# Kernel optimization log

Hardware: AMD Instinct MI355X
Metric: run time of the kernel (lower is better)

## Reference

```python
import jax, jax.numpy as jnp
import numpy as np

LR = 0.1  # inner-loop learning rate from `param - 0.1 * grad`

D = 4096          # memory width d; key/val are (1, d) per docstring
CTX = 512         # loss_context_size: number of keys per update step


def setup_inputs() -> dict:
    key = jax.random.key(0)
    k1, k2, k3 = jax.random.split(key, 3)
    W = jax.random.normal(k1, (D, D), dtype=jnp.float32) / np.sqrt(D)
    keys = jax.random.normal(k2, (CTX, D), dtype=jnp.float32)
    vals = jax.random.normal(k3, (CTX, D), dtype=jnp.float32)
    return {"W": W, "keys": keys, "vals": vals}


def reference(W, keys, vals):
    # OneStep.forward: preds_i = functional_forward(key_i, (W,)) = key_i @ W,
    # loss = MSE(preds, vals); new_W = W - 0.1 * dloss/dW.
    # The per-key loop is batched into a single (CTX, D) x (D, D) matmul.
    def loss_fn(Wp):
        preds = keys @ Wp  # (CTX, D)
        return jnp.mean((preds - vals) ** 2)

    g = jax.grad(loss_fn)(W)
    return W - LR * g
```

## Files before the change

kernel.cpp:

```cpp
#include <hip/hip_runtime.h>
#include <hip/hip_bf16.h>


typedef __bf16 bf16_t;
typedef __bf16 bf16x8 __attribute__((ext_vector_type(8)));
typedef float f32x4 __attribute__((ext_vector_type(4)));

#define D_DIM 4096
#define CTX_N 512
#define UPD_SCALE 9.5367431640625e-8f

__device__ __forceinline__ void gld16(const bf16_t* g, bf16_t* l) {
    __builtin_amdgcn_global_load_lds(
        (const __attribute__((address_space(1))) void*)g,
        (__attribute__((address_space(3))) void*)l, 16, 0, 0);
}

__device__ __forceinline__ void t_body2(
    float* tile, const float* __restrict__ src, bf16_t* __restrict__ dstT,
    bf16_t* __restrict__ dstN, int M, int N, int bx, int by)
{
    const int tid = threadIdx.x;
    const int C0 = bx * 64, R0 = by * 64;
    const int r  = tid >> 2, cs = (tid & 3) * 16;

    const float* s = src + (size_t)(R0 + r) * N + C0 + cs;
    float f[16];
#pragma unroll
    for (int u = 0; u < 4; ++u) {
        const float4 v = ((const float4*)s)[u];
        f[4 * u + 0] = v.x; f[4 * u + 1] = v.y; f[4 * u + 2] = v.z; f[4 * u + 3] = v.w;
    }
#pragma unroll
    for (int u = 0; u < 16; ++u) tile[r * 65 + cs + u] = f[u];

    if (dstN) {
        bf16x8 v0, v1;
#pragma unroll
        for (int u = 0; u < 8; ++u) { v0[u] = (bf16_t)f[u]; v1[u] = (bf16_t)f[8 + u]; }
        bf16_t* d = dstN + (size_t)(R0 + r) * N + C0 + cs;
        *(bf16x8*)d = v0; *(bf16x8*)(d + 8) = v1;
    }
    __syncthreads();

    bf16x8 o0, o1;
#pragma unroll
    for (int u = 0; u < 8; ++u) {
        o0[u] = (bf16_t)tile[(cs + u) * 65 + r];
        o1[u] = (bf16_t)tile[(cs + 8 + u) * 65 + r];
    }
    bf16_t* d = dstT + (size_t)(C0 + r) * M + R0 + cs;
    *(bf16x8*)d = o0; *(bf16x8*)(d + 8) = o1;
}

__global__ __launch_bounds__(256) void t_all(
    const float* __restrict__ W, const float* __restrict__ K,
    const float* __restrict__ V, bf16_t* __restrict__ Wt,
    bf16_t* __restrict__ Kt, bf16_t* __restrict__ Kb, bf16_t* __restrict__ Vt)
{
    __shared__ float tile[64 * 65];
    const int y = blockIdx.y;
    if (y < 64)      t_body2(tile, W, Wt, nullptr, D_DIM, D_DIM, blockIdx.x, y);
    else if (y < 72) t_body2(tile, K, Kt, Kb,      CTX_N, D_DIM, blockIdx.x, y - 64);
    else             t_body2(tile, V, Vt, nullptr, CTX_N, D_DIM, blockIdx.x, y - 72);
}



#define K1_LOAD(AR, BR, T)                                                   \
    _Pragma("unroll")                                                        \
    for (int x = 0; x < 4; ++x) {                                            \
        AR[x] = *(const bf16x8*)(pA + (size_t)(x * 16) * D_DIM + (T) * 32);  \
        BR[x] = *(const bf16x8*)(pB + (size_t)(x * 16) * D_DIM + (T) * 32);  \
    }

#define K1_MFMA(AR, BR)                                                      \
    _Pragma("unroll")                                                        \
    for (int mi = 0; mi < 4; ++mi)                                           \
        _Pragma("unroll")                                                    \
        for (int ni = 0; ni < 4; ++ni)                                       \
            acc[mi][ni] = __builtin_amdgcn_mfma_f32_16x16x32_bf16(           \
                AR[mi], BR[ni], acc[mi][ni], 0, 0, 0);

__global__ __launch_bounds__(256) void k1_residual(
    const bf16_t* __restrict__ Wt, const bf16_t* __restrict__ Kb,
    const bf16_t* __restrict__ Vt, bf16_t* __restrict__ Rt)
{
    __shared__ __align__(16) float ep[64 * 68];

    const int tid = threadIdx.x, wave = tid >> 6, lane = tid & 63;
    const int j0 = blockIdx.x * 64, c0 = blockIdx.y * 64;
    const int l15 = lane & 15, quad = lane >> 4;
    const int kw = wave * 1024;

    f32x4 acc[4][4] = {};

    const bf16_t* pA = Wt + (size_t)(j0 + l15) * D_DIM + kw + quad * 8;
    const bf16_t* pB = Kb + (size_t)(c0 + l15) * D_DIM + kw + quad * 8;

    bf16x8 a0[4], b0[4], a1[4], b1[4], a2[4], b2[4];

    K1_LOAD(a0, b0, 0);
    K1_LOAD(a1, b1, 1);
    K1_LOAD(a2, b2, 2);
#pragma unroll 1
    for (int t = 0; t < 27; t += 3) {
        K1_MFMA(a0, b0); K1_LOAD(a0, b0, t + 3);
        K1_MFMA(a1, b1); K1_LOAD(a1, b1, t + 4);
        K1_MFMA(a2, b2); K1_LOAD(a2, b2, t + 5);
    }
    K1_MFMA(a0, b0); K1_LOAD(a0, b0, 30);
    K1_MFMA(a1, b1); K1_LOAD(a1, b1, 31);
    K1_MFMA(a2, b2);
    K1_MFMA(a0, b0);
    K1_MFMA(a1, b1);

    __syncthreads();
#pragma unroll
    for (int w = 0; w < 4; ++w) {
        if (wave == w) {
#pragma unroll
            for (int mi = 0; mi < 4; ++mi)
#pragma unroll
                for (int ni = 0; ni < 4; ++ni)
#pragma unroll
                    for (int r = 0; r < 4; ++r) {
                        const int row = mi * 16 + quad * 4 + r;
                        const int col = ni * 16 + l15;
                        if (w == 0) ep[row * 68 + col]  = acc[mi][ni][r];
                        else        ep[row * 68 + col] += acc[mi][ni][r];
                    }
        }
        __syncthreads();
    }

    {
        const int row = tid >> 2, cs = (tid & 3) * 16;
        const size_t rbase = (size_t)(j0 + row) * CTX_N + c0 + cs;
        float e[16];
#pragma unroll
        for (int u = 0; u < 4; ++u) {
            const float4 v = ((const float4*)(ep + row * 68 + cs))[u];
            e[4 * u + 0] = v.x; e[4 * u + 1] = v.y;
            e[4 * u + 2] = v.z; e[4 * u + 3] = v.w;
        }
        const bf16x8 v0 = *(const bf16x8*)(Vt + rbase);
        const bf16x8 v1 = *(const bf16x8*)(Vt + rbase + 8);
        bf16x8 o0, o1;
#pragma unroll
        for (int u = 0; u < 8; ++u) {
            o0[u] = (bf16_t)(e[u]     - (float)v0[u]);
            o1[u] = (bf16_t)(e[8 + u] - (float)v1[u]);
        }
        *(bf16x8*)(Rt + rbase)     = o0;
        *(bf16x8*)(Rt + rbase + 8) = o1;
    }
}


#define K2_COMPUTE(BSEL)                                                     \
    {                                                                        \
        const bf16_t* As = (const bf16_t*)(smem + (BSEL) * 16384);           \
        const bf16_t* Bs = (const bf16_t*)(smem + (BSEL) * 16384 + 8192);    \
        bf16x8 af[4], bq[4];                                                 \
        _Pragma("unroll")                                                    \
        for (int mi = 0; mi < 4; ++mi)                                       \
            af[mi] = *(const bf16x8*)(As + (wi + mi * 16 + l15) * 32 + quad * 8); \
        _Pragma("unroll")                                                    \
        for (int ni = 0; ni < 4; ++ni)                                       \
            bq[ni] = *(const bf16x8*)(Bs + (wj + ni * 16 + l15) * 32 + quad * 8); \
        _Pragma("unroll")                                                    \
        for (int mi = 0; mi < 4; ++mi)                                       \
            _Pragma("unroll")                                                \
            for (int ni = 0; ni < 4; ++ni)                                   \
                acc[mi][ni] = __builtin_amdgcn_mfma_f32_16x16x32_bf16(       \
                    af[mi], bq[ni], acc[mi][ni], 0, 0, 0);                   \
    }

__global__ __launch_bounds__(256) void k2_update(
    const bf16_t* __restrict__ Kt, const bf16_t* __restrict__ Rt,
    const float* __restrict__ W, float* __restrict__ out)
{
    __shared__ __align__(16) char smem[32768];

    const int tid = threadIdx.x;

    const int id = blockIdx.x + 32 * blockIdx.y;
    const int xp = (id >> 3) & 31;
    const int yp = (id & 7) + 8 * (id >> 8);
    const int j0 = xp * 128, i0 = yp * 128;

    const int lane = tid & 63, wave = tid >> 6;
    const int wi = (wave >> 1) * 64, wj = (wave & 1) * 64;
    const int l15 = lane & 15, quad = lane >> 4;

    f32x4 acc[4][4] = {};

    const bf16_t* ga = Kt + (size_t)(i0 + (tid >> 2)) * CTX_N + (tid & 3) * 8;
    const bf16_t* gb = Rt + (size_t)(j0 + (tid >> 2)) * CTX_N + (tid & 3) * 8;

    auto stage = [&](int bsel, int cc) {
        bf16_t* la = (bf16_t*)(smem + bsel * 16384) + tid * 8;
        bf16_t* lb = (bf16_t*)(smem + bsel * 16384 + 8192) + tid * 8;
        gld16(ga + cc, la);
        gld16(ga + cc + (size_t)64 * CTX_N, la + 64 * 32);
        gld16(gb + cc, lb);
        gld16(gb + cc + (size_t)64 * CTX_N, lb + 64 * 32);
    };

    stage(0, 0);
    __syncthreads();
#pragma unroll 1
    for (int t = 1; t <= 13; t += 2) {
        stage(1, t * 32);
        __builtin_amdgcn_sched_barrier(0);
        K2_COMPUTE(0);
        __syncthreads();
        stage(0, (t + 1) * 32);
        __builtin_amdgcn_sched_barrier(0);
        K2_COMPUTE(1);
        __syncthreads();
    }
    stage(1, 15 * 32);
    __builtin_amdgcn_sched_barrier(0);
    K2_COMPUTE(0);
    __syncthreads();
    K2_COMPUTE(1);

    const size_t base = (size_t)(i0 + wi + quad * 4) * D_DIM + j0 + wj + l15;
    const float* wp = W + base;
    float*       op = out + base;

    float w0[16], w1[16];
#pragma unroll
    for (int r = 0; r < 4; ++r)
#pragma unroll
        for (int ni = 0; ni < 4; ++ni)
            w0[r * 4 + ni] = wp[(size_t)r * D_DIM + ni * 16];

#pragma unroll
    for (int mi = 0; mi < 4; ++mi) {
        float* wcur = (mi & 1) ? w1 : w0;
        float* wnxt = (mi & 1) ? w0 : w1;
        if (mi < 3) {
#pragma unroll
            for (int r = 0; r < 4; ++r)
#pragma unroll
                for (int ni = 0; ni < 4; ++ni)
                    wnxt[r * 4 + ni] =
                        wp[(size_t)((mi + 1) * 16 + r) * D_DIM + ni * 16];
        }
#pragma unroll
        for (int r = 0; r < 4; ++r)
#pragma unroll
            for (int ni = 0; ni < 4; ++ni)
                op[(size_t)(mi * 16 + r) * D_DIM + ni * 16] =
                    wcur[r * 4 + ni] - UPD_SCALE * acc[mi][ni][r];
    }
}

extern "C" void kernel_launch(void* const* d_in, const int* in_sizes, int n_in,
                              void* d_out, int out_size, void* d_ws, size_t ws_size,
                              hipStream_t stream) {
    const float* W = (const float*)d_in[0];
    const float* K = (const float*)d_in[1];
    const float* V = (const float*)d_in[2];
    float* out = (float*)d_out;

    char* ws = (char*)d_ws;
    bf16_t* Wt = (bf16_t*)(ws);
    bf16_t* Kt = (bf16_t*)(ws + (size_t)32 * 1024 * 1024);
    bf16_t* Kb = (bf16_t*)(ws + (size_t)36 * 1024 * 1024);
    bf16_t* Vt = (bf16_t*)(ws + (size_t)40 * 1024 * 1024);
    bf16_t* Rt = (bf16_t*)(ws + (size_t)44 * 1024 * 1024);

    t_all      <<<dim3(64, 80), 256, 0, stream>>>(W, K, V, Wt, Kt, Kb, Vt);
    k1_residual<<<dim3(64, 8),  256, 0, stream>>>(Wt, Kb, Vt, Rt);
    k2_update  <<<dim3(32, 32), 256, 0, stream>>>(Kt, Rt, W, out);
}
```

Before: 225.6 us.

## Enlarge k1 tile to 128 rows and stage operands via async LDS double buffering

The residual GEMM kernel now computes a 128x64 output tile per block and halves the grid. Operands are fetched with global_load_lds into per-wave double-buffered LDS regions, with explicit waitcnt gating so the next slice's loads overlap the current MFMAs. The aim is to improve operand reuse and hide global load latency. In exchange it uses much more LDS, limiting the kernel to one block per CU, and reduces the number of blocks available to fill the GPU.

```diff
diff --git a/kernel.cpp b/kernel.cpp
--- a/kernel.cpp
+++ b/kernel.cpp
@@ -67,60 +67,96 @@
 
 
 
-#define K1_LOAD(AR, BR, T)                                                   \
-    _Pragma("unroll")                                                        \
-    for (int x = 0; x < 4; ++x) {                                            \
-        AR[x] = *(const bf16x8*)(pA + (size_t)(x * 16) * D_DIM + (T) * 32);  \
-        BR[x] = *(const bf16x8*)(pB + (size_t)(x * 16) * D_DIM + (T) * 32);  \
-    }
-
-#define K1_MFMA(AR, BR)                                                      \
-    _Pragma("unroll")                                                        \
-    for (int mi = 0; mi < 4; ++mi)                                           \
-        _Pragma("unroll")                                                    \
-        for (int ni = 0; ni < 4; ++ni)                                       \
-            acc[mi][ni] = __builtin_amdgcn_mfma_f32_16x16x32_bf16(           \
-                AR[mi], BR[ni], acc[mi][ni], 0, 0, 0);
-
-__global__ __launch_bounds__(256) void k1_residual(
+__global__ __launch_bounds__(256, 1) void k1_residual(
     const bf16_t* __restrict__ Wt, const bf16_t* __restrict__ Kb,
     const bf16_t* __restrict__ Vt, bf16_t* __restrict__ Rt)
 {
-    __shared__ __align__(16) float ep[64 * 68];
+    __shared__ __align__(16) char smem[98304];
 
     const int tid = threadIdx.x, wave = tid >> 6, lane = tid & 63;
-    const int j0 = blockIdx.x * 64, c0 = blockIdx.y * 64;
+    const int j0 = blockIdx.x * 128, c0 = blockIdx.y * 64;
     const int l15 = lane & 15, quad = lane >> 4;
     const int kw = wave * 1024;
 
-    f32x4 acc[4][4] = {};
-
-    const bf16_t* pA = Wt + (size_t)(j0 + l15) * D_DIM + kw + quad * 8;
-    const bf16_t* pB = Kb + (size_t)(c0 + l15) * D_DIM + kw + quad * 8;
-
-    bf16x8 a0[4], b0[4], a1[4], b1[4], a2[4], b2[4];
-
-    K1_LOAD(a0, b0, 0);
-    K1_LOAD(a1, b1, 1);
-    K1_LOAD(a2, b2, 2);
+    bf16_t* reg = (bf16_t*)(smem + wave * 24576);
+
+    f32x4 acc[8][4] = {};
+
+    const bf16_t* ga = Wt + (size_t)(j0 + l15) * D_DIM + kw + quad * 8;
+    const bf16_t* gb = Kb + (size_t)(c0 + l15) * D_DIM + kw + quad * 8;
+
+    auto stageA = [&](int off, int t) {
+        bf16_t* d = reg + off + lane * 8;
+#pragma unroll
+        for (int mi = 0; mi < 8; ++mi)
+            gld16(ga + (size_t)(mi * 16) * D_DIM + t * 32, d + mi * 512);
+    };
+    auto stageB = [&](int off, int t) {
+        bf16_t* d = reg + off + 4096 + lane * 8;
+#pragma unroll
+        for (int ni = 0; ni < 4; ++ni)
+            gld16(gb + (size_t)(ni * 16) * D_DIM + t * 32, d + ni * 512);
+    };
+
+    stageA(0, 0); stageB(0, 0);
 #pragma unroll 1
-    for (int t = 0; t < 27; t += 3) {
-        K1_MFMA(a0, b0); K1_LOAD(a0, b0, t + 3);
-        K1_MFMA(a1, b1); K1_LOAD(a1, b1, t + 4);
-        K1_MFMA(a2, b2); K1_LOAD(a2, b2, t + 5);
-    }
-    K1_MFMA(a0, b0); K1_LOAD(a0, b0, 30);
-    K1_MFMA(a1, b1); K1_LOAD(a1, b1, 31);
-    K1_MFMA(a2, b2);
-    K1_MFMA(a0, b0);
-    K1_MFMA(a1, b1);
-
+    for (int t = 0; t < 31; ++t) {
+        const int cur = (t & 1) ? 6144 : 0;
+        const int nxt = 6144 - cur;
+
+        stageA(nxt, t + 1);
+        __builtin_amdgcn_sched_barrier(0);
+        __builtin_amdgcn_s_waitcnt(0x0f7c);
+        __builtin_amdgcn_sched_barrier(0);
+        bf16x8 a[8];
+#pragma unroll
+        for (int mi = 0; mi < 8; ++mi)
+            a[mi] = *(const bf16x8*)(reg + cur + mi * 512 + lane * 8);
+
+        stageB(nxt, t + 1);
+        __builtin_amdgcn_sched_barrier(0);
+        __builtin_amdgcn_s_waitcnt(0x0f7c);
+        __builtin_amdgcn_sched_barrier(0);
+        bf16x8 b[4];
+#pragma unroll
+        for (int ni = 0; ni < 4; ++ni)
+            b[ni] = *(const bf16x8*)(reg + cur + 4096 + ni * 512 + lane * 8);
+
+#pragma unroll
+        for (int mi = 0; mi < 8; ++mi)
+#pragma unroll
+            for (int ni = 0; ni < 4; ++ni)
+                acc[mi][ni] = __builtin_amdgcn_mfma_f32_16x16x32_bf16(
+                    a[mi], b[ni], acc[mi][ni], 0, 0, 0);
+    }
+    {
+        __builtin_amdgcn_s_waitcnt(0x0f74);
+        __builtin_amdgcn_sched_barrier(0);
+        bf16x8 a[8];
+#pragma unroll
+        for (int mi = 0; mi < 8; ++mi)
+            a[mi] = *(const bf16x8*)(reg + 6144 + mi * 512 + lane * 8);
+        __builtin_amdgcn_s_waitcnt(0x0f70);
+        __builtin_amdgcn_sched_barrier(0);
+        bf16x8 b[4];
+#pragma unroll
+        for (int ni = 0; ni < 4; ++ni)
+            b[ni] = *(const bf16x8*)(reg + 6144 + 4096 + ni * 512 + lane * 8);
+#pragma unroll
+        for (int mi = 0; mi < 8; ++mi)
+#pragma unroll
+            for (int ni = 0; ni < 4; ++ni)
+                acc[mi][ni] = __builtin_amdgcn_mfma_f32_16x16x32_bf16(
+                    a[mi], b[ni], acc[mi][ni], 0, 0, 0);
+    }
+
+    float* ep = (float*)smem;
     __syncthreads();
 #pragma unroll
     for (int w = 0; w < 4; ++w) {
         if (wave == w) {
 #pragma unroll
-            for (int mi = 0; mi < 4; ++mi)
+            for (int mi = 0; mi < 8; ++mi)
 #pragma unroll
                 for (int ni = 0; ni < 4; ++ni)
 #pragma unroll
@@ -135,25 +171,18 @@
     }
 
     {
-        const int row = tid >> 2, cs = (tid & 3) * 16;
+        const int row = tid >> 1, cs = (tid & 1) * 32;
         const size_t rbase = (size_t)(j0 + row) * CTX_N + c0 + cs;
-        float e[16];
+        const float* erow = ep + row * 68 + cs;
 #pragma unroll
         for (int u = 0; u < 4; ++u) {
-            const float4 v = ((const float4*)(ep + row * 68 + cs))[u];
-            e[4 * u + 0] = v.x; e[4 * u + 1] = v.y;
-            e[4 * u + 2] = v.z; e[4 * u + 3] = v.w;
+            const bf16x8 vv = *(const bf16x8*)(Vt + rbase + u * 8);
+            bf16x8 o;
+#pragma unroll
+            for (int j = 0; j < 8; ++j)
+                o[j] = (bf16_t)(erow[u * 8 + j] - (float)vv[j]);
+            *(bf16x8*)(Rt + rbase + u * 8) = o;
         }
-        const bf16x8 v0 = *(const bf16x8*)(Vt + rbase);
-        const bf16x8 v1 = *(const bf16x8*)(Vt + rbase + 8);
-        bf16x8 o0, o1;
-#pragma unroll
-        for (int u = 0; u < 8; ++u) {
-            o0[u] = (bf16_t)(e[u]     - (float)v0[u]);
-            o1[u] = (bf16_t)(e[8 + u] - (float)v1[u]);
-        }
-        *(bf16x8*)(Rt + rbase)     = o0;
-        *(bf16x8*)(Rt + rbase + 8) = o1;
     }
 }
 
@@ -275,6 +304,6 @@
     bf16_t* Rt = (bf16_t*)(ws + (size_t)44 * 1024 * 1024);
 
     t_all      <<<dim3(64, 80), 256, 0, stream>>>(W, K, V, Wt, Kt, Kb, Vt);
-    k1_residual<<<dim3(64, 8),  256, 0, stream>>>(Wt, Kb, Vt, Rt);
+    k1_residual<<<dim3(32, 8),  256, 0, stream>>>(Wt, Kb, Vt, Rt);
     k2_update  <<<dim3(32, 32), 256, 0, stream>>>(Kt, Rt, W, out);
 }
```

New measurement: 217.1 us. -3.8%, faster.

## Restructure residual GEMM into LDS double-buffered 128x64 tiles with 8 waves

Applied to the files above, without the earlier changes.

The residual kernel previously split the K dimension across 4 waves, had each wave load directly from global memory into registers, and reduced the partial results through shared memory. It now uses 512-thread blocks covering 128x64 output tiles. Operands are staged into double-buffered LDS with global_load_lds, and each wave owns a 32x32 sub-tile over the full K range. This removes the cross-wave split-K reduction and lets waves share operand loads through LDS. In exchange it adds a barrier on every K step, halves the grid to 256 blocks, and writes the epilogue as scalar bf16 stores that do not coalesce well.

```diff
diff --git a/kernel.cpp b/kernel.cpp
--- a/kernel.cpp
+++ b/kernel.cpp
@@ -67,93 +67,87 @@
 
 
 
-#define K1_LOAD(AR, BR, T)                                                   \
-    _Pragma("unroll")                                                        \
-    for (int x = 0; x < 4; ++x) {                                            \
-        AR[x] = *(const bf16x8*)(pA + (size_t)(x * 16) * D_DIM + (T) * 32);  \
-        BR[x] = *(const bf16x8*)(pB + (size_t)(x * 16) * D_DIM + (T) * 32);  \
-    }
-
-#define K1_MFMA(AR, BR)                                                      \
-    _Pragma("unroll")                                                        \
-    for (int mi = 0; mi < 4; ++mi)                                           \
-        _Pragma("unroll")                                                    \
-        for (int ni = 0; ni < 4; ++ni)                                       \
-            acc[mi][ni] = __builtin_amdgcn_mfma_f32_16x16x32_bf16(           \
-                AR[mi], BR[ni], acc[mi][ni], 0, 0, 0);
-
-__global__ __launch_bounds__(256) void k1_residual(
+__global__ __launch_bounds__(512, 2) void k1_residual(
     const bf16_t* __restrict__ Wt, const bf16_t* __restrict__ Kb,
     const bf16_t* __restrict__ Vt, bf16_t* __restrict__ Rt)
 {
-    __shared__ __align__(16) float ep[64 * 68];
+    __shared__ __align__(16) bf16_t stg[2 * 12288];
 
     const int tid = threadIdx.x, wave = tid >> 6, lane = tid & 63;
-    const int j0 = blockIdx.x * 64, c0 = blockIdx.y * 64;
+    const int j0 = blockIdx.x * 128, c0 = blockIdx.y * 64;
     const int l15 = lane & 15, quad = lane >> 4;
-    const int kw = wave * 1024;
-
-    f32x4 acc[4][4] = {};
-
-    const bf16_t* pA = Wt + (size_t)(j0 + l15) * D_DIM + kw + quad * 8;
-    const bf16_t* pB = Kb + (size_t)(c0 + l15) * D_DIM + kw + quad * 8;
-
-    bf16x8 a0[4], b0[4], a1[4], b1[4], a2[4], b2[4];
-
-    K1_LOAD(a0, b0, 0);
-    K1_LOAD(a1, b1, 1);
-    K1_LOAD(a2, b2, 2);
+    const int wm = wave >> 1, wn = wave & 1;
+
+    f32x4 acc[2][2] = {};
+
+    const int smi = wave >> 1, skk = wave & 1;
+    const bf16_t* gA1 = Wt + (size_t)(j0 + smi * 16 + l15) * D_DIM + skk * 32 + quad * 8;
+    const bf16_t* gA2 = gA1 + (size_t)64 * D_DIM;
+    const bf16_t* gB  = Kb + (size_t)(c0 + smi * 16 + l15) * D_DIM + skk * 32 + quad * 8;
+
+    auto stage = [&](int bsel, int t) {
+        bf16_t* base = stg + bsel * 12288;
+        gld16(gA1 + t * 64, base + (size_t)wave * 512 + lane * 8);
+        gld16(gA2 + t * 64, base + (size_t)(8 + wave) * 512 + lane * 8);
+        gld16(gB  + t * 64, base + 8192 + (size_t)wave * 512 + lane * 8);
+    };
+
+#define K1_COMPUTE(BSEL)                                                     \
+    {                                                                        \
+        const bf16_t* buf = stg + (BSEL) * 12288;                            \
+        bf16x8 a[2][2], b[2][2];                                             \
+        _Pragma("unroll")                                                    \
+        for (int kk = 0; kk < 2; ++kk)                                       \
+            _Pragma("unroll")                                                \
+            for (int x = 0; x < 2; ++x) {                                    \
+                a[x][kk] = *(const bf16x8*)(                                 \
+                    buf + ((wm * 2 + x) * 2 + kk) * 512 + lane * 8);         \
+                b[x][kk] = *(const bf16x8*)(                                 \
+                    buf + 8192 + ((wn * 2 + x) * 2 + kk) * 512 + lane * 8);  \
+            }                                                                \
+        _Pragma("unroll")                                                    \
+        for (int kk = 0; kk < 2; ++kk)                                       \
+            _Pragma("unroll")                                                \
+            for (int mi = 0; mi < 2; ++mi)                                   \
+                _Pragma("unroll")                                            \
+                for (int ni = 0; ni < 2; ++ni)                               \
+                    acc[mi][ni] = __builtin_amdgcn_mfma_f32_16x16x32_bf16(   \
+                        a[mi][kk], b[ni][kk], acc[mi][ni], 0, 0, 0);         \
+    }
+
+    stage(0, 0);
+    __syncthreads();
 #pragma unroll 1
-    for (int t = 0; t < 27; t += 3) {
-        K1_MFMA(a0, b0); K1_LOAD(a0, b0, t + 3);
-        K1_MFMA(a1, b1); K1_LOAD(a1, b1, t + 4);
-        K1_MFMA(a2, b2); K1_LOAD(a2, b2, t + 5);
-    }
-    K1_MFMA(a0, b0); K1_LOAD(a0, b0, 30);
-    K1_MFMA(a1, b1); K1_LOAD(a1, b1, 31);
-    K1_MFMA(a2, b2);
-    K1_MFMA(a0, b0);
-    K1_MFMA(a1, b1);
-
-    __syncthreads();
-#pragma unroll
-    for (int w = 0; w < 4; ++w) {
-        if (wave == w) {
-#pragma unroll
-            for (int mi = 0; mi < 4; ++mi)
-#pragma unroll
-                for (int ni = 0; ni < 4; ++ni)
-#pragma unroll
-                    for (int r = 0; r < 4; ++r) {
-                        const int row = mi * 16 + quad * 4 + r;
-                        const int col = ni * 16 + l15;
-                        if (w == 0) ep[row * 68 + col]  = acc[mi][ni][r];
-                        else        ep[row * 68 + col] += acc[mi][ni][r];
-                    }
-        }
-        __syncthreads();
-    }
+    for (int t = 0; t < 62; t += 2) {
+        stage(1, t + 1);
+        __builtin_amdgcn_sched_barrier(0);
+        K1_COMPUTE(0);
+        __syncthreads();
+        stage(0, t + 2);
+        __builtin_amdgcn_sched_barrier(0);
+        K1_COMPUTE(1);
+        __syncthreads();
+    }
+    stage(1, 63);
+    __builtin_amdgcn_sched_barrier(0);
+    K1_COMPUTE(0);
+    __syncthreads();
+    K1_COMPUTE(1);
 
     {
-        const int row = tid >> 2, cs = (tid & 3) * 16;
-        const size_t rbase = (size_t)(j0 + row) * CTX_N + c0 + cs;
-        float e[16];
-#pragma unroll
-        for (int u = 0; u < 4; ++u) {
-            const float4 v = ((const float4*)(ep + row * 68 + cs))[u];
-            e[4 * u + 0] = v.x; e[4 * u + 1] = v.y;
-            e[4 * u + 2] = v.z; e[4 * u + 3] = v.w;
-        }
-        const bf16x8 v0 = *(const bf16x8*)(Vt + rbase);
-        const bf16x8 v1 = *(const bf16x8*)(Vt + rbase + 8);
-        bf16x8 o0, o1;
-#pragma unroll
-        for (int u = 0; u < 8; ++u) {
-            o0[u] = (bf16_t)(e[u]     - (float)v0[u]);
-            o1[u] = (bf16_t)(e[8 + u] - (float)v1[u]);
-        }
-        *(bf16x8*)(Rt + rbase)     = o0;
-        *(bf16x8*)(Rt + rbase + 8) = o1;
+        const size_t base =
+            (size_t)(j0 + wm * 32 + quad * 4) * CTX_N + c0 + wn * 32 + l15;
+#pragma unroll
+        for (int mi = 0; mi < 2; ++mi)
+#pragma unroll
+            for (int r = 0; r < 4; ++r) {
+                const size_t rowb = base + (size_t)(mi * 16 + r) * CTX_N;
+#pragma unroll
+                for (int ni = 0; ni < 2; ++ni) {
+                    const size_t idx = rowb + ni * 16;
+                    Rt[idx] = (bf16_t)(acc[mi][ni][r] - (float)Vt[idx]);
+                }
+            }
     }
 }
 
@@ -275,6 +269,6 @@
     bf16_t* Rt = (bf16_t*)(ws + (size_t)44 * 1024 * 1024);
 
     t_all      <<<dim3(64, 80), 256, 0, stream>>>(W, K, V, Wt, Kt, Kb, Vt);
-    k1_residual<<<dim3(64, 8),  256, 0, stream>>>(Wt, Kb, Vt, Rt);
+    k1_residual<<<dim3(32, 8),  512, 0, stream>>>(Wt, Kb, Vt, Rt);
     k2_update  <<<dim3(32, 32), 256, 0, stream>>>(Kt, Rt, W, out);
 }
```

New measurement: 228.0 us. No clear change (+1.1%).
